# Kernel tuning notes

Measured on AMD Instinct MI355X. Metric: run time of the kernel, lower is better.

Reference implementation:

```python
import jax, jax.numpy as jnp
import numpy as np

B, S, D, H = 8, 1024, 512, 8
HD = D // H
EPS = 1e-5


def layer_norm(x, g, b):
    m = jnp.mean(x, axis=-1, keepdims=True)
    v = jnp.mean(jnp.square(x - m), axis=-1, keepdims=True)
    return (x - m) * jax.lax.rsqrt(v + EPS) * g + b


def mha(x, w_in, b_in, w_out, b_out):
    # x: [B,S,D]; w_in: [3D,D]; PyTorch MultiheadAttention math (no dropout, eval)
    b, s, d = x.shape
    qkv = x @ w_in.T + b_in                      # [B,S,3D]
    q, k, v = jnp.split(qkv, 3, axis=-1)
    q = q.reshape(b, s, H, HD)
    k = k.reshape(b, s, H, HD)
    v = v.reshape(b, s, H, HD)
    scores = jnp.einsum('bqhd,bkhd->bhqk', q, k) / np.sqrt(HD)
    a = jax.nn.softmax(scores, axis=-1)
    o = jnp.einsum('bhqk,bkhd->bqhd', a, v).reshape(b, s, d)
    return o @ w_out.T + b_out


def interp_linear(y, out_size):
    # y: [B,S_in,D]; torch F.interpolate(mode='linear', align_corners=False)
    s_in = y.shape[1]
    scale = s_in / out_size
    src = (jnp.arange(out_size, dtype=jnp.float32) + 0.5) * scale - 0.5
    src = jnp.clip(src, 0.0, s_in - 1.0)
    i0 = jnp.floor(src).astype(jnp.int32)
    i1 = jnp.minimum(i0 + 1, s_in - 1)
    w = (src - i0.astype(jnp.float32))[None, :, None]
    return y[:, i0, :] * (1.0 - w) + y[:, i1, :] * w


def setup_inputs() -> dict:
    key = jax.random.key(0)
    ks = jax.random.split(key, 16)
    sd = 0.02
    return {
        'x': jax.random.normal(ks[0], (B, S, D), jnp.float32),
        'w_in1': jax.random.normal(ks[1], (3 * D, D), jnp.float32) * sd,
        'b_in1': jnp.zeros((3 * D,), jnp.float32),
        'w_out1': jax.random.normal(ks[2], (D, D), jnp.float32) * sd,
        'b_out1': jnp.zeros((D,), jnp.float32),
        'w_in2': jax.random.normal(ks[3], (3 * D, D), jnp.float32) * sd,
        'b_in2': jnp.zeros((3 * D,), jnp.float32),
        'w_out2': jax.random.normal(ks[4], (D, D), jnp.float32) * sd,
        'b_out2': jnp.zeros((D,), jnp.float32),
        'g1': jnp.ones((D,), jnp.float32), 'beta1': jnp.zeros((D,), jnp.float32),
        'g2': jnp.ones((D,), jnp.float32), 'beta2': jnp.zeros((D,), jnp.float32),
        'g3': jnp.ones((D,), jnp.float32), 'beta3': jnp.zeros((D,), jnp.float32),
        'w_ff1': jax.random.normal(ks[5], (4 * D, D), jnp.float32) * sd,
        'b_ff1': jnp.zeros((4 * D,), jnp.float32),
        'w_ff2': jax.random.normal(ks[6], (D, 4 * D), jnp.float32) * sd,
        'b_ff2': jnp.zeros((D,), jnp.float32),
    }


def reference(x, w_in1, b_in1, w_out1, b_out1, w_in2, b_in2, w_out2, b_out2,
              g1, beta1, g2, beta2, g3, beta3, w_ff1, b_ff1, w_ff2, b_ff2):
    a1 = mha(x, w_in1, b_in1, w_out1, b_out1)
    x = layer_norm(x + a1, g1, beta1)
    # avg_pool1d kernel=2 stride=2 ceil_mode (S even -> exact halving)
    pooled = x.reshape(B, S // 2, 2, D).mean(axis=2)
    a2 = mha(pooled, w_in2, b_in2, w_out2, b_out2)
    up = interp_linear(a2, S)
    x = layer_norm(x + up, g2, beta2)
    h = jax.nn.gelu(x @ w_ff1.T + b_ff1, approximate=False)
    ff = h @ w_ff2.T + b_ff2
    return layer_norm(x + ff, g3, beta3)
```

## Files before the change

### kernel.cpp

```cpp
#include <hip/hip_runtime.h>
#include <hip/hip_bf16.h>
#include <math.h>

typedef __hip_bfloat16 bf16;
typedef __attribute__((ext_vector_type(8))) short short8;
typedef __attribute__((ext_vector_type(4))) float f32x4;
typedef __attribute__((ext_vector_type(16))) float f32x16;

__device__ __forceinline__ float ldf(const float* p, size_t i) { return p[i]; }
__device__ __forceinline__ float ldf(const bf16*  p, size_t i) { return __bfloat162float(p[i]); }
__device__ __forceinline__ void  stf(float* p, size_t i, float v) { p[i] = v; }
__device__ __forceinline__ void  stf(bf16*  p, size_t i, float v) { p[i] = __float2bfloat16(v); }

__device__ __forceinline__ float ex2(float x) { return __builtin_amdgcn_exp2f(x); }

__device__ __forceinline__ float gelu_f(float x) {
    float u = 0.7978845608f * (x + 0.044715f * x * x * x);
    float e = ex2(u * 2.885390082f);
    float t = 1.0f - 2.0f / (e + 1.0f);
    return 0.5f * x * (1.0f + t);
}

__device__ __forceinline__ void gl16(const void* gp, void* lp) {
    __builtin_amdgcn_global_load_lds(
        (const __attribute__((address_space(1))) void*)gp,
        (__attribute__((address_space(3))) void*)lp, 16, 0, 0);
}

__device__ __forceinline__ void pl32swap(unsigned &a, unsigned &b) {
    asm volatile("v_permlane32_swap_b32 %0, %1" : "+v"(a), "+v"(b));
}

__global__ __launch_bounds__(256) void cvt_all(
    const float* __restrict__ x,
    const float* __restrict__ s0, const float* __restrict__ s1,
    const float* __restrict__ s2, const float* __restrict__ s3,
    const float* __restrict__ s4, const float* __restrict__ s5,
    bf16* __restrict__ dst)
{
    int i = blockIdx.x * 256 + threadIdx.x;
    if (i < 4194304) {
        dst[i] = __float2bfloat16(x[i]);
        return;
    }
    int j = i - 4194304;
    const float* s; int off;
    if      (j <  786432) { s = s0; off = 0; }
    else if (j < 1048576) { s = s1; off =  786432; }
    else if (j < 1835008) { s = s2; off = 1048576; }
    else if (j < 2097152) { s = s3; off = 1835008; }
    else if (j < 3145728) { s = s4; off = 2097152; }
    else                  { s = s5; off = 3145728; }
    dst[i] = __float2bfloat16(s[j - off]);
}

template <int EPI, int BN, int VS>
__global__ __launch_bounds__(256) void gemm_rs(
    const bf16* __restrict__ A, const bf16* __restrict__ W,
    const float* __restrict__ bias, bf16* __restrict__ C,
    bf16* __restrict__ vt, int M, int N, int K)
{
    constexpr int WNC = BN / 2;
    constexpr int NT  = BN / 32;
    constexpr int RB  = BN / 32;

    __shared__ __align__(16) bf16 Asl[128 * 64];
    __shared__ __align__(16) bf16 Bsl[BN * 64];

    const int tid  = threadIdx.x;
    const int lane = tid & 63;
    const int wave = tid >> 6;
    const int wm   = wave >> 1, wn = wave & 1;
    const int l15  = lane & 15, quad = lane >> 4;

    const int nwg = gridDim.x * gridDim.y;
    const int bid = blockIdx.y * gridDim.x + blockIdx.x;
    const int wid = (bid & 7) * (nwg >> 3) + (bid >> 3);
    const int bx  = wid % gridDim.x, by = wid / gridDim.x;
    const int row0 = by * 128, col0 = bx * BN;

    const int sr = tid >> 3;
    const int gg = tid & 7;

    const bf16* As[4]; const bf16* Ws[RB]; int loA[4], loB[RB];
    #pragma unroll
    for (int j = 0; j < 4; j++) {
        int row = j * 32 + sr;
        int gs  = (gg ^ (row & 7)) * 8;
        As[j]  = &A[(size_t)(row0 + row) * K + gs];
        loA[j] = row * 64 + gg * 8;
    }
    #pragma unroll
    for (int j = 0; j < RB; j++) {
        int row = j * 32 + sr;
        int gs  = (gg ^ (row & 7)) * 8;
        Ws[j]  = &W[(size_t)(col0 + row) * K + gs];
        loB[j] = row * 64 + gg * 8;
    }

    short8 ga[4], gb[RB];
    auto LOADG = [&](int k0) {
        #pragma unroll
        for (int j = 0; j < 4; j++) ga[j] = *(const short8*)(As[j] + k0);
        #pragma unroll
        for (int j = 0; j < RB; j++) gb[j] = *(const short8*)(Ws[j] + k0);
    };
    auto WRITEL = [&]() {
        #pragma unroll
        for (int j = 0; j < 4; j++) *(short8*)&Asl[loA[j]] = ga[j];
        #pragma unroll
        for (int j = 0; j < RB; j++) *(short8*)&Bsl[loB[j]] = gb[j];
    };

    f32x4 acc[4][NT] = {};
    const int nk = K >> 6;

    LOADG(0);
    WRITEL();
    __syncthreads();

    for (int i = 0; i < nk; i++) {
        if (i + 1 < nk) LOADG((i + 1) << 6);

        #pragma unroll
        for (int ks = 0; ks < 64; ks += 32) {
            short8 af[4], bfr[NT];
            const int g0 = (ks >> 3) + quad;
            const int col = (g0 ^ (l15 & 7)) * 8;
            #pragma unroll
            for (int mt = 0; mt < 4; mt++)
                af[mt] = *(const short8*)&Asl[(wm * 64 + mt * 16 + l15) * 64 + col];
            #pragma unroll
            for (int nt = 0; nt < NT; nt++)
                bfr[nt] = *(const short8*)&Bsl[(wn * WNC + nt * 16 + l15) * 64 + col];
            #pragma unroll
            for (int mt = 0; mt < 4; mt++)
                #pragma unroll
                for (int nt = 0; nt < NT; nt++)
                    acc[mt][nt] = __builtin_amdgcn_mfma_f32_16x16x32_bf16(
                        af[mt], bfr[nt], acc[mt][nt], 0, 0, 0);
        }

        if (i + 1 < nk) {
            __syncthreads();
            WRITEL();
            __syncthreads();
        }
    }

    if constexpr (VS > 0) {
        if (col0 >= 1024) {
            constexpr int LS = (VS == 1024) ? 10 : 9;
            #pragma unroll
            for (int mt = 0; mt < 4; mt++) {
                int rowm = row0 + wm * 64 + mt * 16 + quad * 4;
                int b8 = rowm >> LS;
                int s4 = rowm & (VS - 1);
                #pragma unroll
                for (int nt = 0; nt < NT; nt++) {
                    int col = col0 + wn * WNC + nt * 16 + l15;
                    float bv = bias[col];
                    int hd = col - 1024;
                    union { bf16 b4[4]; unsigned long long u; } pk;
                    #pragma unroll
                    for (int r = 0; r < 4; r++)
                        pk.b4[r] = __float2bfloat16(acc[mt][nt][r] + bv);
                    *(unsigned long long*)&vt[
                        ((size_t)(b8 * 8 + (hd >> 6)) * 64 + (hd & 63)) * VS + s4] = pk.u;
                }
            }
            return;
        }
    }

    #pragma unroll
    for (int mt = 0; mt < 4; mt++) {
        int row = row0 + wm * 64 + mt * 16 + quad * 4;
        #pragma unroll
        for (int nt = 0; nt < NT; nt++) {
            int col = col0 + wn * WNC + nt * 16 + l15;
            float bv = bias[col];
            #pragma unroll
            for (int r = 0; r < 4; r++) {
                float v = acc[mt][nt][r] + bv;
                if (EPI == 1) v = gelu_f(v);
                C[(size_t)(row + r) * N + col] = __float2bfloat16(v);
            }
        }
    }
}

template <int LQB>
__global__ __launch_bounds__(128) void flash_attn_mfma(
    const bf16* __restrict__ qkv, const bf16* __restrict__ vt,
    bf16* __restrict__ o)
{
    constexpr int S  = 64 << LQB;
    constexpr int nt = 1 << LQB;

    __shared__ __align__(16) bf16 Kl[2][64 * 64];
    __shared__ __align__(16) bf16 Vl[2][64 * 64];

    const int tid  = threadIdx.x;
    const int wave = tid >> 6, lane = tid & 63;
    const int l31  = lane & 31, hi = lane >> 5;

    const int r    = blockIdx.x;
    const int w    = (r & 7) * ((1 << LQB) * 8) + (r >> 3);
    const int qblk = w & ((1 << LQB) - 1);
    const int bh   = w >> LQB;
    const int h    = bh & 7, bb = bh >> 3;
    const int q0   = qblk * 64 + wave * 32;

    const bf16* base  = qkv + (size_t)bb * S * 1536 + h * 64;
    const bf16* vbase = vt + (size_t)bh * 64 * S;

    short8 qf[4];
    #pragma unroll
    for (int c = 0; c < 4; c++)
        qf[c] = *(const short8*)&base[(size_t)(q0 + l31) * 1536 + c * 16 + hi * 8];

    const int sr = lane >> 3;
    const int sc = ((lane & 7) ^ sr) * 8;

    auto STGKV = [&](int buf, int k0) {
        #pragma unroll
        for (int t = 0; t < 4; t++) {
            int r0 = wave * 32 + t * 8;
            gl16(&base[(size_t)(k0 + r0 + sr) * 1536 + 512 + sc], &Kl[buf][r0 * 64]);
        }
        #pragma unroll
        for (int t = 0; t < 4; t++) {
            int r0 = wave * 32 + t * 8;
            gl16(&vbase[(size_t)(r0 + sr) * S + k0 + sc], &Vl[buf][r0 * 64]);
        }
    };

    f32x16 oacc[2] = {};
    float lrow = 0.f;
    const float CE = 0.18033688f;

    STGKV(0, 0);

    for (int it = 0; it < nt; it++) {
        const int cur = it & 1;
        __syncthreads();
        if (it + 1 < nt) STGKV(cur ^ 1, (it + 1) << 6);

        const bf16* Kc = &Kl[cur][0];
        const bf16* Vc = &Vl[cur][0];
        #pragma unroll
        for (int sub = 0; sub < 2; sub++) {
            f32x16 st = {};
            #pragma unroll
            for (int c = 0; c < 4; c++) {
                const int row  = sub * 32 + l31;
                const int slot = (c * 2 + hi) ^ (row & 7);
                short8 af = *(const short8*)&Kc[row * 64 + slot * 8];
                st = __builtin_amdgcn_mfma_f32_32x32x16_bf16(af, qf[c], st, 0, 0, 0);
            }

            float p[16]; float ps = 0.f;
            #pragma unroll
            for (int r2 = 0; r2 < 16; r2++) {
                p[r2] = ex2(st[r2] * CE - 2.0f);
                ps += p[r2];
            }
            lrow += ps;

            unsigned wk[8];
            #pragma unroll
            for (int jj = 0; jj < 8; jj++)
                asm("v_cvt_pk_bf16_f32 %0, %1, %2"
                    : "=v"(wk[jj]) : "v"(p[2*jj]), "v"(p[2*jj+1]));

            #pragma unroll
            for (int kk = 0; kk < 2; kk++) {
                pl32swap(wk[kk*4+0], wk[kk*4+2]);
                pl32swap(wk[kk*4+1], wk[kk*4+3]);
                union { unsigned u[4]; short8 s; } pa;
                pa.u[0] = wk[kk*4+0]; pa.u[1] = wk[kk*4+1];
                pa.u[2] = wk[kk*4+2]; pa.u[3] = wk[kk*4+3];
                #pragma unroll
                for (int dt = 0; dt < 2; dt++) {
                    const int row  = dt * 32 + l31;
                    const int slot = (sub * 4 + kk * 2 + hi) ^ (row & 7);
                    short8 vf = *(const short8*)&Vc[row * 64 + slot * 8];
                    oacc[dt] = __builtin_amdgcn_mfma_f32_32x32x16_bf16(
                        pa.s, vf, oacc[dt], 0, 0, 0);
                }
            }
        }
    }

    lrow += __shfl_xor(lrow, 32);
    float inv = 1.0f / lrow;
    #pragma unroll
    for (int r2 = 0; r2 < 16; r2++) {
        int qr = (r2 & 3) + 8 * (r2 >> 2) + 4 * hi;
        float iv = __shfl(inv, qr);
        size_t rb = ((size_t)bb * S + q0 + qr) * 512 + h * 64;
        o[rb + l31]      = __float2bfloat16(oacc[0][r2] * iv);
        o[rb + 32 + l31] = __float2bfloat16(oacc[1][r2] * iv);
    }
}

template <typename AT, typename OT, bool INTERP>
__global__ __launch_bounds__(256) void ln_kernel(
    const AT* __restrict__ a, const bf16* __restrict__ bsrc,
    const float* __restrict__ g, const float* __restrict__ beta,
    OT* __restrict__ out)
{
    const int row = blockIdx.x;
    const int t = threadIdx.x;
    const size_t base = (size_t)row * 512;

    float a0 = ldf(a, base + t), a1 = ldf(a, base + t + 256);
    float b0, b1;
    if (INTERP) {
        int s = row & 1023, bb = row >> 10;
        float src = fminf(fmaxf((s + 0.5f) * 0.5f - 0.5f, 0.f), 511.f);
        int i0 = (int)src;
        int i1 = min(i0 + 1, 511);
        float w = src - (float)i0;
        size_t r0 = ((size_t)bb * 512 + i0) * 512;
        size_t r1 = ((size_t)bb * 512 + i1) * 512;
        b0 = __bfloat162float(bsrc[r0 + t]) * (1.f - w) + __bfloat162float(bsrc[r1 + t]) * w;
        b1 = __bfloat162float(bsrc[r0 + t + 256]) * (1.f - w) + __bfloat162float(bsrc[r1 + t + 256]) * w;
    } else {
        b0 = __bfloat162float(bsrc[base + t]);
        b1 = __bfloat162float(bsrc[base + t + 256]);
    }
    float v0 = a0 + b0, v1 = a1 + b1;

    __shared__ float red[4];
    const int lane = t & 63, wid = t >> 6;

    float sm = v0 + v1;
    #pragma unroll
    for (int off = 32; off > 0; off >>= 1) sm += __shfl_xor(sm, off);
    if (lane == 0) red[wid] = sm;
    __syncthreads();
    sm = red[0] + red[1] + red[2] + red[3];
    const float mean = sm * (1.0f / 512.0f);

    float d0 = v0 - mean, d1 = v1 - mean;
    float vv = d0 * d0 + d1 * d1;
    __syncthreads();
    #pragma unroll
    for (int off = 32; off > 0; off >>= 1) vv += __shfl_xor(vv, off);
    if (lane == 0) red[wid] = vv;
    __syncthreads();
    vv = red[0] + red[1] + red[2] + red[3];
    const float rstd = rsqrtf(vv * (1.0f / 512.0f) + 1e-5f);

    stf(out, base + t,       d0 * rstd * g[t]       + beta[t]);
    stf(out, base + t + 256, d1 * rstd * g[t + 256] + beta[t + 256]);
}

__global__ __launch_bounds__(256) void ln_pool_kernel(
    const float* __restrict__ a, const bf16* __restrict__ bsrc,
    const float* __restrict__ g, const float* __restrict__ beta,
    bf16* __restrict__ x1, bf16* __restrict__ pooled)
{
    const int pr = blockIdx.x;
    const int t = threadIdx.x;
    const size_t base0 = (size_t)(2 * pr) * 512;
    const size_t base1 = base0 + 512;

    float u0 = a[base0 + t]       + __bfloat162float(bsrc[base0 + t]);
    float u1 = a[base0 + t + 256] + __bfloat162float(bsrc[base0 + t + 256]);
    float w0 = a[base1 + t]       + __bfloat162float(bsrc[base1 + t]);
    float w1 = a[base1 + t + 256] + __bfloat162float(bsrc[base1 + t + 256]);

    __shared__ float red[2][4];
    const int lane = t & 63, wid = t >> 6;

    float s0 = u0 + u1, s1 = w0 + w1;
    #pragma unroll
    for (int off = 32; off > 0; off >>= 1) {
        s0 += __shfl_xor(s0, off);
        s1 += __shfl_xor(s1, off);
    }
    if (lane == 0) { red[0][wid] = s0; red[1][wid] = s1; }
    __syncthreads();
    const float m0 = (red[0][0] + red[0][1] + red[0][2] + red[0][3]) * (1.0f / 512.0f);
    const float m1 = (red[1][0] + red[1][1] + red[1][2] + red[1][3]) * (1.0f / 512.0f);

    float du0 = u0 - m0, du1 = u1 - m0, dw0 = w0 - m1, dw1 = w1 - m1;
    float v0 = du0 * du0 + du1 * du1, v1 = dw0 * dw0 + dw1 * dw1;
    __syncthreads();
    #pragma unroll
    for (int off = 32; off > 0; off >>= 1) {
        v0 += __shfl_xor(v0, off);
        v1 += __shfl_xor(v1, off);
    }
    if (lane == 0) { red[0][wid] = v0; red[1][wid] = v1; }
    __syncthreads();
    const float r0 = rsqrtf((red[0][0] + red[0][1] + red[0][2] + red[0][3]) * (1.0f / 512.0f) + 1e-5f);
    const float r1 = rsqrtf((red[1][0] + red[1][1] + red[1][2] + red[1][3]) * (1.0f / 512.0f) + 1e-5f);

    float g0 = g[t], g1v = g[t + 256], be0 = beta[t], be1 = beta[t + 256];
    float y00 = du0 * r0 * g0  + be0;
    float y01 = du1 * r0 * g1v + be1;
    float y10 = dw0 * r1 * g0  + be0;
    float y11 = dw1 * r1 * g1v + be1;

    x1[base0 + t]       = __float2bfloat16(y00);
    x1[base0 + t + 256] = __float2bfloat16(y01);
    x1[base1 + t]       = __float2bfloat16(y10);
    x1[base1 + t + 256] = __float2bfloat16(y11);

    const size_t pb = (size_t)pr * 512;
    pooled[pb + t]       = __float2bfloat16(0.5f * (y00 + y10));
    pooled[pb + t + 256] = __float2bfloat16(0.5f * (y01 + y11));
}

extern "C" void kernel_launch(void* const* d_in, const int* in_sizes, int n_in,
                              void* d_out, int out_size, void* d_ws, size_t ws_size,
                              hipStream_t stream)
{
    const float* x      = (const float*)d_in[0];
    const float* w_in1  = (const float*)d_in[1];
    const float* b_in1  = (const float*)d_in[2];
    const float* w_out1 = (const float*)d_in[3];
    const float* b_out1 = (const float*)d_in[4];
    const float* w_in2  = (const float*)d_in[5];
    const float* b_in2  = (const float*)d_in[6];
    const float* w_out2 = (const float*)d_in[7];
    const float* b_out2 = (const float*)d_in[8];
    const float* g1     = (const float*)d_in[9];
    const float* be1    = (const float*)d_in[10];
    const float* g2     = (const float*)d_in[11];
    const float* be2    = (const float*)d_in[12];
    const float* g3     = (const float*)d_in[13];
    const float* be3    = (const float*)d_in[14];
    const float* w_ff1  = (const float*)d_in[15];
    const float* b_ff1  = (const float*)d_in[16];
    const float* w_ff2  = (const float*)d_in[17];
    const float* b_ff2  = (const float*)d_in[18];

    bf16* ws     = (bf16*)d_ws;
    bf16* xb     = ws + 0;
    bf16* wq1    = ws + 4194304;
    bf16* wo1    = ws + 4980736;
    bf16* wq2    = ws + 5242880;
    bf16* wo2    = ws + 6029312;
    bf16* wf1    = ws + 6291456;
    bf16* wf2    = ws + 7340032;
    bf16* qkv1   = ws + 8388608;
    bf16* o1     = ws + 20971520;
    bf16* a1     = ws + 25165824;
    bf16* x1     = ws + 29360128;
    bf16* pooled = ws + 33554432;
    bf16* qkv2   = ws + 35651584;
    bf16* o2     = ws + 41943040;
    bf16* a2     = ws + 44040192;
    bf16* x2     = ws + 46137344;
    bf16* h      = ws + 8388608;
    bf16* ff     = ws + 25165824;
    bf16* vt     = ws + 46137344;

    dim3 blk(256);
    dim3 fblk(128);

    cvt_all<<<32768, blk, 0, stream>>>(x, w_in1, w_out1, w_in2, w_out2, w_ff1, w_ff2, xb);

    gemm_rs<0,128,1024><<<dim3(12, 64), blk, 0, stream>>>(xb, wq1, b_in1, qkv1, vt, 8192, 1536, 512);
    flash_attn_mfma<4><<<dim3(1024), fblk, 0, stream>>>(qkv1, vt, o1);
    gemm_rs<0,64,0><<<dim3(8, 64), blk, 0, stream>>>(o1, wo1, b_out1, a1, nullptr, 8192, 512, 512);
    ln_pool_kernel<<<4096, blk, 0, stream>>>(x, a1, g1, be1, x1, pooled);
    gemm_rs<0,64,512><<<dim3(24, 32), blk, 0, stream>>>(pooled, wq2, b_in2, qkv2, vt, 4096, 1536, 512);
    flash_attn_mfma<3><<<dim3(512), fblk, 0, stream>>>(qkv2, vt, o2);
    gemm_rs<0,64,0><<<dim3(8, 32), blk, 0, stream>>>(o2, wo2, b_out2, a2, nullptr, 4096, 512, 512);
    ln_kernel<bf16, bf16, true><<<8192, blk, 0, stream>>>(x1, a2, g2, be2, x2);
    gemm_rs<1,128,0><<<dim3(16, 64), blk, 0, stream>>>(x2, wf1, b_ff1, h, nullptr, 8192, 2048, 512);
    gemm_rs<0,64,0><<<dim3(8, 64), blk, 0, stream>>>(h, wf2, b_ff2, ff, nullptr, 8192, 512, 2048);
    ln_kernel<bf16, float, false><<<8192, blk, 0, stream>>>(x2, ff, g3, be3, (float*)d_out);
}
```

Baseline: 303.4 us.

## Fuse fp32-to-bf16 conversion into GEMM operand loads, drop cvt_all kernel

Removes the standalone conversion kernel that cast the input and all weights to bf16. The GEMM kernel is templated on operand type, so fp32 operands are loaded as 8-float vectors and converted to bf16 in registers before the LDS store. This saves a launch and a full write-then-read of the converted buffers. In exchange each GEMM tile reads twice the global bytes for fp32 weights, which are re-read by many blocks, and uses more registers for the staging vectors.

```diff
diff --git a/kernel.cpp b/kernel.cpp
--- a/kernel.cpp
+++ b/kernel.cpp
@@ -4,6 +4,7 @@
 
 typedef __hip_bfloat16 bf16;
 typedef __attribute__((ext_vector_type(8))) short short8;
+typedef __attribute__((ext_vector_type(8))) float f32x8;
 typedef __attribute__((ext_vector_type(4))) float f32x4;
 typedef __attribute__((ext_vector_type(16))) float f32x16;
 
@@ -31,32 +32,24 @@
     asm volatile("v_permlane32_swap_b32 %0, %1" : "+v"(a), "+v"(b));
 }
 
-__global__ __launch_bounds__(256) void cvt_all(
-    const float* __restrict__ x,
-    const float* __restrict__ s0, const float* __restrict__ s1,
-    const float* __restrict__ s2, const float* __restrict__ s3,
-    const float* __restrict__ s4, const float* __restrict__ s5,
-    bf16* __restrict__ dst)
-{
-    int i = blockIdx.x * 256 + threadIdx.x;
-    if (i < 4194304) {
-        dst[i] = __float2bfloat16(x[i]);
-        return;
-    }
-    int j = i - 4194304;
-    const float* s; int off;
-    if      (j <  786432) { s = s0; off = 0; }
-    else if (j < 1048576) { s = s1; off =  786432; }
-    else if (j < 1835008) { s = s2; off = 1048576; }
-    else if (j < 2097152) { s = s3; off = 1835008; }
-    else if (j < 3145728) { s = s4; off = 2097152; }
-    else                  { s = s5; off = 3145728; }
-    dst[i] = __float2bfloat16(s[j - off]);
-}
-
-template <int EPI, int BN, int VS>
+template <typename T> struct VecT { using R = short8; };
+template <>           struct VecT<float> { using R = f32x8; };
+
+__device__ __forceinline__ short8 to_bf8(short8 v) { return v; }
+__device__ __forceinline__ short8 to_bf8(f32x8 v) {
+    short8 r;
+    #pragma unroll
+    for (int e = 0; e < 8; e++) {
+        union { bf16 b; short s; } cv;
+        cv.b = __float2bfloat16(v[e]);
+        r[e] = cv.s;
+    }
+    return r;
+}
+
+template <int EPI, int BN, int VS, typename TA, typename TW>
 __global__ __launch_bounds__(256) void gemm_rs(
-    const bf16* __restrict__ A, const bf16* __restrict__ W,
+    const TA* __restrict__ A, const TW* __restrict__ W,
     const float* __restrict__ bias, bf16* __restrict__ C,
     bf16* __restrict__ vt, int M, int N, int K)
 {
@@ -82,7 +75,7 @@
     const int sr = tid >> 3;
     const int gg = tid & 7;
 
-    const bf16* As[4]; const bf16* Ws[RB]; int loA[4], loB[RB];
+    const TA* As[4]; const TW* Ws[RB]; int loA[4], loB[RB];
     #pragma unroll
     for (int j = 0; j < 4; j++) {
         int row = j * 32 + sr;
@@ -98,18 +91,21 @@
         loB[j] = row * 64 + gg * 8;
     }
 
-    short8 ga[4], gb[RB];
+    typename VecT<TA>::R ga[4];
+    typename VecT<TW>::R gb[RB];
     auto LOADG = [&](int k0) {
         #pragma unroll
-        for (int j = 0; j < 4; j++) ga[j] = *(const short8*)(As[j] + k0);
-        #pragma unroll
-        for (int j = 0; j < RB; j++) gb[j] = *(const short8*)(Ws[j] + k0);
+        for (int j = 0; j < 4; j++)
+            ga[j] = *(const typename VecT<TA>::R*)(As[j] + k0);
+        #pragma unroll
+        for (int j = 0; j < RB; j++)
+            gb[j] = *(const typename VecT<TW>::R*)(Ws[j] + k0);
     };
     auto WRITEL = [&]() {
         #pragma unroll
-        for (int j = 0; j < 4; j++) *(short8*)&Asl[loA[j]] = ga[j];
-        #pragma unroll
-        for (int j = 0; j < RB; j++) *(short8*)&Bsl[loB[j]] = gb[j];
+        for (int j = 0; j < 4; j++) *(short8*)&Asl[loA[j]] = to_bf8(ga[j]);
+        #pragma unroll
+        for (int j = 0; j < RB; j++) *(short8*)&Bsl[loB[j]] = to_bf8(gb[j]);
     };
 
     f32x4 acc[4][NT] = {};
@@ -441,13 +437,6 @@
     const float* b_ff2  = (const float*)d_in[18];
 
     bf16* ws     = (bf16*)d_ws;
-    bf16* xb     = ws + 0;
-    bf16* wq1    = ws + 4194304;
-    bf16* wo1    = ws + 4980736;
-    bf16* wq2    = ws + 5242880;
-    bf16* wo2    = ws + 6029312;
-    bf16* wf1    = ws + 6291456;
-    bf16* wf2    = ws + 7340032;
     bf16* qkv1   = ws + 8388608;
     bf16* o1     = ws + 20971520;
     bf16* a1     = ws + 25165824;
@@ -464,17 +453,21 @@
     dim3 blk(256);
     dim3 fblk(128);
 
-    cvt_all<<<32768, blk, 0, stream>>>(x, w_in1, w_out1, w_in2, w_out2, w_ff1, w_ff2, xb);
-
-    gemm_rs<0,128,1024><<<dim3(12, 64), blk, 0, stream>>>(xb, wq1, b_in1, qkv1, vt, 8192, 1536, 512);
+    gemm_rs<0,128,1024, float, float><<<dim3(12, 64), blk, 0, stream>>>(
+        x, w_in1, b_in1, qkv1, vt, 8192, 1536, 512);
     flash_attn_mfma<4><<<dim3(1024), fblk, 0, stream>>>(qkv1, vt, o1);
-    gemm_rs<0,64,0><<<dim3(8, 64), blk, 0, stream>>>(o1, wo1, b_out1, a1, nullptr, 8192, 512, 512);
+    gemm_rs<0,64,0, bf16, float><<<dim3(8, 64), blk, 0, stream>>>(
+        o1, w_out1, b_out1, a1, nullptr, 8192, 512, 512);
     ln_pool_kernel<<<4096, blk, 0, stream>>>(x, a1, g1, be1, x1, pooled);
-    gemm_rs<0,64,512><<<dim3(24, 32), blk, 0, stream>>>(pooled, wq2, b_in2, qkv2, vt, 4096, 1536, 512);
+    gemm_rs<0,64,512, bf16, float><<<dim3(24, 32), blk, 0, stream>>>(
+        pooled, w_in2, b_in2, qkv2, vt, 4096, 1536, 512);
     flash_attn_mfma<3><<<dim3(512), fblk, 0, stream>>>(qkv2, vt, o2);
-    gemm_rs<0,64,0><<<dim3(8, 32), blk, 0, stream>>>(o2, wo2, b_out2, a2, nullptr, 4096, 512, 512);
+    gemm_rs<0,64,0, bf16, float><<<dim3(8, 32), blk, 0, stream>>>(
+        o2, w_out2, b_out2, a2, nullptr, 4096, 512, 512);
     ln_kernel<bf16, bf16, true><<<8192, blk, 0, stream>>>(x1, a2, g2, be2, x2);
-    gemm_rs<1,128,0><<<dim3(16, 64), blk, 0, stream>>>(x2, wf1, b_ff1, h, nullptr, 8192, 2048, 512);
-    gemm_rs<0,64,0><<<dim3(8, 64), blk, 0, stream>>>(h, wf2, b_ff2, ff, nullptr, 8192, 512, 2048);
+    gemm_rs<1,128,0, bf16, float><<<dim3(16, 64), blk, 0, stream>>>(
+        x2, w_ff1, b_ff1, h, nullptr, 8192, 2048, 512);
+    gemm_rs<0,64,0, bf16, float><<<dim3(8, 64), blk, 0, stream>>>(
+        h, w_ff2, b_ff2, ff, nullptr, 8192, 512, 2048);
     ln_kernel<bf16, float, false><<<8192, blk, 0, stream>>>(x2, ff, g3, be3, (float*)d_out);
 }
```

After: 312.4 us. 1.03x slower.
